# Optimization experiments

Measured on AMD Instinct MI355X. Metric: run time of the kernel, lower is better.

## Reference

```python
import jax, jax.numpy as jnp
import numpy as np
import math

D_MODEL = 1024
N_HEADS = 16
HEAD_DIM = D_MODEL // N_HEADS  # 64
R = HEAD_DIM // 2              # 32
ROPE_BASE = 10000.0
B, T = 4, 2048


def setup_inputs() -> dict:
    key = jax.random.key(0)
    k1, k2, k3, k4, k5 = jax.random.split(key, 5)
    x = jax.random.normal(k1, (B, T, D_MODEL), dtype=jnp.float32)
    Wqkv = jax.random.normal(k2, (3 * D_MODEL, D_MODEL), dtype=jnp.float32) * (1.0 / math.sqrt(D_MODEL))
    Wout = jax.random.normal(k3, (D_MODEL, D_MODEL), dtype=jnp.float32) * (1.0 / math.sqrt(D_MODEL))
    alpha = jax.random.normal(k4, (N_HEADS, R), dtype=jnp.float32) * 0.01
    beta = jax.random.normal(k5, (N_HEADS, R), dtype=jnp.float32) * 0.01
    return {"x": x, "Wqkv": Wqkv, "Wout": Wout, "alpha": alpha, "beta": beta}


def _fourier_bias(alpha, beta, t):
    # omega[r] = base^{-2r/head_dim}, same geometric spacing as RoPE
    omega = ROPE_BASE ** (-2.0 * jnp.arange(R, dtype=jnp.float32) / HEAD_DIM)
    # bias depends only on displacement i-j in [-(t-1), t-1]: compute once per
    # displacement, then gather into the (t, t) matrix (same math as full T x T).
    disp = jnp.arange(-(t - 1), t, dtype=jnp.float32)            # (2t-1,)
    angles = omega[:, None] * disp[None, :]                       # (R, 2t-1)
    vec = jnp.einsum('hr,rk->hk', alpha, jnp.cos(angles)) \
        + jnp.einsum('hr,rk->hk', beta, jnp.sin(angles))          # (H, 2t-1)
    i = jnp.arange(t)
    idx = i[:, None] - i[None, :] + (t - 1)                       # (t, t), delta[i,j]=i-j
    return vec[:, idx]                                            # (H, t, t)


def reference(x, Wqkv, Wout, alpha, beta):
    b, t, d = x.shape
    qkv = x @ Wqkv.T                                              # (B, T, 3D)
    q, k, v = jnp.split(qkv, 3, axis=-1)
    def heads(a):
        return a.reshape(b, t, N_HEADS, HEAD_DIM).transpose(0, 2, 1, 3)  # (B,H,T,dh)
    q, k, v = heads(q), heads(k), heads(v)
    scale = 1.0 / math.sqrt(HEAD_DIM)
    logits = jnp.einsum('bhqd,bhkd->bhqk', q, k) * scale          # (B,H,T,T)
    logits = logits + _fourier_bias(alpha, beta, t)[None]
    causal = jnp.tril(jnp.ones((t, t), dtype=bool))
    logits = jnp.where(causal[None, None], logits, -jnp.inf)
    attn = jax.nn.softmax(logits, axis=-1)
    out = jnp.einsum('bhqk,bhkd->bhqd', attn, v)                  # (B,H,T,dh)
    out = out.transpose(0, 2, 1, 3).reshape(b, t, d)
    return out @ Wout.T
```

## Files before the change

kernel.cpp:

```cpp
#include <hip/hip_runtime.h>
#include <cstdint>
#include <cstddef>

typedef _Float16 f16;
typedef f16 f16x8 __attribute__((ext_vector_type(8)));
typedef __fp16 fp16x2 __attribute__((ext_vector_type(2)));
typedef float f32x4 __attribute__((ext_vector_type(4)));
typedef float f32x16 __attribute__((ext_vector_type(16)));
typedef uint32_t u32;


__device__ __forceinline__ void gload16(const void* g, void* l) {
  __builtin_amdgcn_global_load_lds((const __attribute__((address_space(1))) void*)g,
                                   (__attribute__((address_space(3))) void*)l,
                                   16u, 0, 0u);
}

__device__ __forceinline__ u32 pkrtz(float a, float b) {
  union { fp16x2 v; u32 u; } t;
  t.v = __builtin_amdgcn_cvt_pkrtz(a, b);
  return t.u;
}

__device__ __forceinline__ u32 packh2(float a, float b) { return pkrtz(a, b); }

__device__ __forceinline__ float max3f(float a, float b, float c) {
  return fmaxf(fmaxf(a, b), c);
}

__device__ __forceinline__ void pl32swap(u32& a, u32& b) {
  asm volatile("v_permlane32_swap_b32 %0, %1" : "+v"(a), "+v"(b));
}


__global__ __launch_bounds__(256) void cvt_f32_f16(const float* __restrict__ in,
                                                   f16* __restrict__ out, int n) {
  int i = (blockIdx.x * 256 + threadIdx.x) * 8;
  if (i >= n) return;
  float4 a = *(const float4*)(in + i);
  float4 b = *(const float4*)(in + i + 4);
  f16x8 o;
  o[0] = (f16)a.x; o[1] = (f16)a.y; o[2] = (f16)a.z; o[3] = (f16)a.w;
  o[4] = (f16)b.x; o[5] = (f16)b.y; o[6] = (f16)b.z; o[7] = (f16)b.w;
  *(f16x8*)(out + i) = o;
}


__global__ __launch_bounds__(256) void build_tables(const float* __restrict__ alpha,
                                                    const float* __restrict__ beta,
                                                    f16* __restrict__ U,
                                                    f16* __restrict__ Wt) {
  int idx = blockIdx.x * 256 + threadIdx.x;
  int t = idx >> 5, r = idx & 31;
  float w = powf(10000.0f, -(float)r / 32.0f);
  float ang = w * (float)t;
  float c = cosf(ang), s = sinf(ang);
  const float L2E = 1.44269504089f;
  U[t * 64 + 2 * r]     = (f16)(c * L2E);
  U[t * 64 + 2 * r + 1] = (f16)(s * L2E);
  #pragma unroll
  for (int h = 0; h < 16; ++h) {
    float al = alpha[h * 32 + r], be = beta[h * 32 + r];
    Wt[(size_t)(h * 2048 + t) * 64 + 2 * r]     = (f16)(al * c - be * s);
    Wt[(size_t)(h * 2048 + t) * 64 + 2 * r + 1] = (f16)(al * s + be * c);
  }
}


__global__ __launch_bounds__(256) void gemm_qkv(const f16* __restrict__ A,
                                                const f16* __restrict__ B,
                                                f16* __restrict__ Q,
                                                f16* __restrict__ Kh,
                                                f16* __restrict__ Vt) {
  __shared__ __align__(16) char sm[65536];
  const int K = 1024;
  int tid = threadIdx.x;
  int lane = tid & 63, wid = tid >> 6;
  int bid = blockIdx.x;
  int xcd = bid & 7;
  int id = bid >> 3;
  int nl = id / 64;
  int m0 = (id & 63) * 128;
  int n0 = (xcd * 3 + nl) * 128;
  int wm = wid >> 1, wn = wid & 1;
  int c = lane & 15, g = lane >> 4, l7 = lane & 7;

  int srow[4], sce[4], sdst[4];
  #pragma unroll
  for (int i = 0; i < 4; ++i) {
    int p = i * 4096 + tid * 16;
    int q = p ^ (((p >> 7) & 7) << 4);
    srow[i] = q >> 7; sce[i] = (q & 127) >> 1;
    sdst[i] = i * 4096 + wid * 1024;
  }

  f32x4 acc[4][4] = {};

  #pragma unroll
  for (int i = 0; i < 4; ++i) {
    gload16(A + (size_t)(m0 + srow[i]) * K + sce[i], sm + sdst[i]);
    gload16(B + (size_t)(n0 + srow[i]) * K + sce[i], sm + 32768 + sdst[i]);
  }
  __syncthreads();

  for (int kt = 0; kt < 16; ++kt) {
    int cur = kt & 1;
    char* As = sm + cur * 16384;
    char* Bs = sm + 32768 + cur * 16384;

    if (kt < 15) {
      char* Ad = sm + (cur ^ 1) * 16384;
      char* Bd = sm + 32768 + (cur ^ 1) * 16384;
      #pragma unroll
      for (int i = 0; i < 4; ++i) {
        gload16(A + (size_t)(m0 + srow[i]) * K + (kt + 1) * 64 + sce[i], Ad + sdst[i]);
        gload16(B + (size_t)(n0 + srow[i]) * K + (kt + 1) * 64 + sce[i], Bd + sdst[i]);
      }
    }

    __builtin_amdgcn_s_setprio(1);
    #pragma unroll
    for (int kk = 0; kk < 2; ++kk) {
      int co = (kk * 64 + g * 16) ^ (l7 << 4);
      f16x8 af[4], bf[4];
      #pragma unroll
      for (int fr = 0; fr < 4; ++fr)
        af[fr] = *(const f16x8*)(As + (wm * 64 + fr * 16 + c) * 128 + co);
      #pragma unroll
      for (int fn = 0; fn < 4; ++fn)
        bf[fn] = *(const f16x8*)(Bs + (wn * 64 + fn * 16 + c) * 128 + co);
      #pragma unroll
      for (int fr = 0; fr < 4; ++fr)
        #pragma unroll
        for (int fn = 0; fn < 4; ++fn)
          acc[fr][fn] = __builtin_amdgcn_mfma_f32_16x16x32_f16(af[fr], bf[fn], acc[fr][fn], 0, 0, 0);
    }
    __builtin_amdgcn_s_setprio(0);
    __syncthreads();
  }

  int which = n0 >> 10;
  #pragma unroll
  for (int fr = 0; fr < 4; ++fr) {
    int m = m0 + wm * 64 + fr * 16 + g * 4;
    int b = m >> 11, t = m & 2047;
    #pragma unroll
    for (int fn = 0; fn < 4; ++fn) {
      int n = n0 + wn * 64 + fn * 16 + c;
      int nf = n & 1023, hh = nf >> 6, d = nf & 63;
      if (which == 0) {
        #pragma unroll
        for (int r = 0; r < 4; ++r)
          Q[(size_t)((b * 16 + hh) * 2048 + (t + r)) * 64 + d] = (f16)(acc[fr][fn][r] * 0.180336880111f);
      } else if (which == 1) {
        #pragma unroll
        for (int r = 0; r < 4; ++r)
          Kh[(size_t)((b * 16 + hh) * 2048 + (t + r)) * 64 + d] = (f16)acc[fr][fn][r];
      } else {
        uint2 pk;
        pk.x = packh2(acc[fr][fn][0], acc[fr][fn][1]);
        pk.y = packh2(acc[fr][fn][2], acc[fr][fn][3]);
        *(uint2*)(Vt + (size_t)((b * 16 + hh) * 64 + d) * 2048 + t) = pk;
      }
    }
  }
}


__global__ __launch_bounds__(256) void gemm_out(const f16* __restrict__ A,
                                                const f16* __restrict__ B,
                                                float* __restrict__ Cout) {
  __shared__ __align__(16) char sm[65536];
  const int K = 1024;
  int tid = threadIdx.x;
  int lane = tid & 63, wid = tid >> 6;
  int bid = blockIdx.x;
  int xcd = bid & 7;
  int id = bid >> 3;
  int m0 = id * 128;
  int n0 = xcd * 128;
  int wm = wid >> 1, wn = wid & 1;
  int c = lane & 15, g = lane >> 4, l7 = lane & 7;

  int srow[4], sce[4], sdst[4];
  #pragma unroll
  for (int i = 0; i < 4; ++i) {
    int p = i * 4096 + tid * 16;
    int q = p ^ (((p >> 7) & 7) << 4);
    srow[i] = q >> 7; sce[i] = (q & 127) >> 1;
    sdst[i] = i * 4096 + wid * 1024;
  }

  f32x4 acc[4][4] = {};

  #pragma unroll
  for (int i = 0; i < 4; ++i) {
    gload16(A + (size_t)(m0 + srow[i]) * K + sce[i], sm + sdst[i]);
    gload16(B + (size_t)(n0 + srow[i]) * K + sce[i], sm + 32768 + sdst[i]);
  }
  __syncthreads();

  for (int kt = 0; kt < 16; ++kt) {
    int cur = kt & 1;
    char* As = sm + cur * 16384;
    char* Bs = sm + 32768 + cur * 16384;

    if (kt < 15) {
      char* Ad = sm + (cur ^ 1) * 16384;
      char* Bd = sm + 32768 + (cur ^ 1) * 16384;
      #pragma unroll
      for (int i = 0; i < 4; ++i) {
        gload16(A + (size_t)(m0 + srow[i]) * K + (kt + 1) * 64 + sce[i], Ad + sdst[i]);
        gload16(B + (size_t)(n0 + srow[i]) * K + (kt + 1) * 64 + sce[i], Bd + sdst[i]);
      }
    }

    __builtin_amdgcn_s_setprio(1);
    #pragma unroll
    for (int kk = 0; kk < 2; ++kk) {
      int co = (kk * 64 + g * 16) ^ (l7 << 4);
      f16x8 af[4], bf[4];
      #pragma unroll
      for (int fr = 0; fr < 4; ++fr)
        af[fr] = *(const f16x8*)(As + (wm * 64 + fr * 16 + c) * 128 + co);
      #pragma unroll
      for (int fn = 0; fn < 4; ++fn)
        bf[fn] = *(const f16x8*)(Bs + (wn * 64 + fn * 16 + c) * 128 + co);
      #pragma unroll
      for (int fr = 0; fr < 4; ++fr)
        #pragma unroll
        for (int fn = 0; fn < 4; ++fn)
          acc[fr][fn] = __builtin_amdgcn_mfma_f32_16x16x32_f16(af[fr], bf[fn], acc[fr][fn], 0, 0, 0);
    }
    __builtin_amdgcn_s_setprio(0);
    __syncthreads();
  }

  #pragma unroll
  for (int fr = 0; fr < 4; ++fr) {
    int m = m0 + wm * 64 + fr * 16 + g * 4;
    #pragma unroll
    for (int fn = 0; fn < 4; ++fn) {
      int n = n0 + wn * 64 + fn * 16 + c;
      #pragma unroll
      for (int r = 0; r < 4; ++r)
        Cout[(size_t)(m + r) * 1024 + n] = acc[fr][fn][r];
    }
  }
}


__global__ __launch_bounds__(512, 2) void attn(const f16* __restrict__ Q,
                                               const f16* __restrict__ Kh,
                                               const f16* __restrict__ Vt,
                                               const f16* __restrict__ U,
                                               const f16* __restrict__ Wt,
                                               f16* __restrict__ AO) {
  __shared__ __align__(16) char sm[98304];
  int tid = threadIdx.x, lane = tid & 63, wid = tid >> 6;
  int l31 = lane & 31, hi = lane >> 5;
  int o = blockIdx.x;
  int pr = o >> 6;
  int bh = o & 63;
  int h = bh & 15, b = bh >> 4;
  int swz = (lane & 15) << 4;

  const f16* ksrc[4]; int kdst[4];
  #pragma unroll
  for (int i = 0; i < 4; ++i) {
    int p = i * 8192 + tid * 16;
    int row = p >> 8;
    int col = (p & 255) ^ ((row & 15) << 4);
    int ce = col >> 1;
    ksrc[i] = (ce < 64) ? (Kh + (size_t)(bh * 2048 + row) * 64 + ce)
                        : (Wt + (size_t)(h * 2048 + row) * 64 + (ce - 64));
    kdst[i] = i * 8192 + wid * 1024;
  }
  const f16* vsrc[2]; int vdst[2];
  #pragma unroll
  for (int i = 0; i < 2; ++i) {
    int p = i * 8192 + tid * 16;
    int row = p >> 8;
    int col = (p & 255) ^ ((row & 15) << 4);
    int ce = col >> 1;
    vsrc[i] = Vt + (size_t)(bh * 64 + row) * 2048 + ce;
    vdst[i] = i * 8192 + wid * 1024;
  }

  #pragma unroll 1
  for (int pass = 0; pass < 2; ++pass) {
    int qt = pass ? pr : 7 - pr;
    int qrow = qt * 256 + wid * 32 + l31;
    int ktmax = 2 * qt + 1;

    f16x8 qf[8];
    {
      const f16* qp = Q + (size_t)(bh * 2048 + qrow) * 64 + hi * 8;
      const f16* up = U + (size_t)qrow * 64 + hi * 8;
      #pragma unroll
      for (int ks = 0; ks < 4; ++ks) {
        qf[ks]     = *(const f16x8*)(qp + ks * 16);
        qf[4 + ks] = *(const f16x8*)(up + ks * 16);
      }
    }

    float m_i = -1e30f, l_i = 0.0f;
    f32x16 accA = {}, accB = {};

    #pragma unroll
    for (int i = 0; i < 4; ++i) gload16(ksrc[i], sm + kdst[i]);
    #pragma unroll
    for (int i = 0; i < 2; ++i) gload16(vsrc[i], sm + 65536 + vdst[i]);
    __syncthreads();

    for (int kt = 0; kt <= ktmax; ++kt) {
      int cur = kt & 1;
      char* Ks = sm + cur * 32768;
      char* Vs = sm + 65536 + cur * 16384;

      if (kt < ktmax) {
        char* kb = sm + (cur ^ 1) * 32768;
        char* vb = sm + 65536 + (cur ^ 1) * 16384;
        #pragma unroll
        for (int i = 0; i < 4; ++i) gload16(ksrc[i] + (size_t)(kt + 1) * 8192, kb + kdst[i]);
        #pragma unroll
        for (int i = 0; i < 2; ++i) gload16(vsrc[i] + (size_t)(kt + 1) * 128, vb + vdst[i]);
      }

      f32x16 st0 = {}, st1 = {}, st2 = {}, st3 = {};
      __builtin_amdgcn_s_setprio(1);
      #pragma unroll
      for (int ks = 0; ks < 8; ++ks) {
        int co = (ks * 32 + hi * 16) ^ swz;
        f16x8 k0 = *(const f16x8*)(Ks + l31 * 256 + co);
        f16x8 k1 = *(const f16x8*)(Ks + (32 + l31) * 256 + co);
        f16x8 k2 = *(const f16x8*)(Ks + (64 + l31) * 256 + co);
        f16x8 k3 = *(const f16x8*)(Ks + (96 + l31) * 256 + co);
        st0 = __builtin_amdgcn_mfma_f32_32x32x16_f16(k0, qf[ks], st0, 0, 0, 0);
        st1 = __builtin_amdgcn_mfma_f32_32x32x16_f16(k1, qf[ks], st1, 0, 0, 0);
        st2 = __builtin_amdgcn_mfma_f32_32x32x16_f16(k2, qf[ks], st2, 0, 0, 0);
        st3 = __builtin_amdgcn_mfma_f32_32x32x16_f16(k3, qf[ks], st3, 0, 0, 0);
      }
      __builtin_amdgcn_s_setprio(0);

      int kv0 = kt * 128;
      if (kv0 + 127 > qt * 256 + wid * 32) {
        #pragma unroll
        for (int r = 0; r < 16; ++r) {
          int kvl = kv0 + (r & 3) + 8 * (r >> 2) + 4 * hi;
          if (kvl > qrow) st0[r] = -1e30f;
          if (kvl + 32 > qrow) st1[r] = -1e30f;
          if (kvl + 64 > qrow) st2[r] = -1e30f;
          if (kvl + 96 > qrow) st3[r] = -1e30f;
        }
      }

      float pm = fmaxf(fmaxf(st0[0], st1[0]), fmaxf(st2[0], st3[0]));
      #pragma unroll
      for (int r = 1; r < 16; ++r) {
        pm = max3f(pm, st0[r], st1[r]);
        pm = max3f(pm, st2[r], st3[r]);
      }
      pm = fmaxf(pm, __shfl_xor(pm, 32, 64));
      if (!__all(pm <= m_i + 8.0f)) {
        float mnew = fmaxf(m_i, pm);
        float sc = __builtin_amdgcn_exp2f(m_i - mnew);
        l_i *= sc;
        accA *= sc;
        accB *= sc;
        m_i = mnew;
      }

      float ps = 0.0f;
      u32 pk0[8], pk1[8], pk2[8], pk3[8];
      #pragma unroll
      for (int j = 0; j < 8; ++j) {
        float a0 = __builtin_amdgcn_exp2f(st0[2 * j] - m_i);
        float a1 = __builtin_amdgcn_exp2f(st0[2 * j + 1] - m_i);
        float b0 = __builtin_amdgcn_exp2f(st1[2 * j] - m_i);
        float b1 = __builtin_amdgcn_exp2f(st1[2 * j + 1] - m_i);
        float c0 = __builtin_amdgcn_exp2f(st2[2 * j] - m_i);
        float c1 = __builtin_amdgcn_exp2f(st2[2 * j + 1] - m_i);
        float d0 = __builtin_amdgcn_exp2f(st3[2 * j] - m_i);
        float d1 = __builtin_amdgcn_exp2f(st3[2 * j + 1] - m_i);
        ps += (a0 + a1) + (b0 + b1) + (c0 + c1) + (d0 + d1);
        pk0[j] = pkrtz(a0, a1);
        pk1[j] = pkrtz(b0, b1);
        pk2[j] = pkrtz(c0, c1);
        pk3[j] = pkrtz(d0, d1);
      }
      ps += __shfl_xor(ps, 32, 64);
      l_i += ps;

      pl32swap(pk0[0], pk0[2]); pl32swap(pk0[1], pk0[3]);
      pl32swap(pk0[4], pk0[6]); pl32swap(pk0[5], pk0[7]);
      pl32swap(pk1[0], pk1[2]); pl32swap(pk1[1], pk1[3]);
      pl32swap(pk1[4], pk1[6]); pl32swap(pk1[5], pk1[7]);
      pl32swap(pk2[0], pk2[2]); pl32swap(pk2[1], pk2[3]);
      pl32swap(pk2[4], pk2[6]); pl32swap(pk2[5], pk2[7]);
      pl32swap(pk3[0], pk3[2]); pl32swap(pk3[1], pk3[3]);
      pl32swap(pk3[4], pk3[6]); pl32swap(pk3[5], pk3[7]);

      __builtin_amdgcn_s_setprio(1);
      #pragma unroll
      for (int kb = 0; kb < 8; ++kb) {
        union { u32 w[4]; f16x8 v; } bf;
        const u32* pk = (kb < 2) ? pk0 : (kb < 4) ? pk1 : (kb < 6) ? pk2 : pk3;
        int base = (kb & 1) * 4;
        bf.w[0] = pk[base + 0]; bf.w[1] = pk[base + 1];
        bf.w[2] = pk[base + 2]; bf.w[3] = pk[base + 3];
        int co = (kb * 32 + hi * 16) ^ swz;
        f16x8 v0 = *(const f16x8*)(Vs + l31 * 256 + co);
        f16x8 v1 = *(const f16x8*)(Vs + (32 + l31) * 256 + co);
        accA = __builtin_amdgcn_mfma_f32_32x32x16_f16(v0, bf.v, accA, 0, 0, 0);
        accB = __builtin_amdgcn_mfma_f32_32x32x16_f16(v1, bf.v, accB, 0, 0, 0);
      }
      __builtin_amdgcn_s_setprio(0);
      __syncthreads();
    }

    float inv = __builtin_amdgcn_rcpf(l_i);
    f16* aop = AO + (size_t)(b * 2048 + qrow) * 1024 + h * 64;
    #pragma unroll
    for (int u = 0; u < 4; ++u) {
      uint2 ov;
      ov.x = pkrtz(accA[4 * u] * inv, accA[4 * u + 1] * inv);
      ov.y = pkrtz(accA[4 * u + 2] * inv, accA[4 * u + 3] * inv);
      *(uint2*)(aop + 8 * u + 4 * hi) = ov;
      ov.x = pkrtz(accB[4 * u] * inv, accB[4 * u + 1] * inv);
      ov.y = pkrtz(accB[4 * u + 2] * inv, accB[4 * u + 3] * inv);
      *(uint2*)(aop + 32 + 8 * u + 4 * hi) = ov;
    }
  }
}


extern "C" void kernel_launch(void* const* d_in, const int* in_sizes, int n_in,
                              void* d_out, int out_size, void* d_ws, size_t ws_size,
                              hipStream_t stream) {
  const float* x     = (const float*)d_in[0];
  const float* Wqkv  = (const float*)d_in[1];
  const float* Wout  = (const float*)d_in[2];
  const float* alpha = (const float*)d_in[3];
  const float* beta  = (const float*)d_in[4];

  char* ws = (char*)d_ws;
  f16* Xh    = (f16*)(ws);
  f16* Wqkvh = (f16*)(ws + 16777216);
  f16* Wouth = (f16*)(ws + 23068672);
  f16* Qh    = (f16*)(ws + 25165824);
  f16* Kh    = (f16*)(ws + 41943040);
  f16* Vt    = (f16*)(ws + 58720256);
  f16* U     = (f16*)(ws + 75497472);
  f16* Wt    = (f16*)(ws + 75759616);
  f16* AO    = Xh;

  cvt_f32_f16<<<4096, 256, 0, stream>>>(x, Xh, 8388608);
  cvt_f32_f16<<<1536, 256, 0, stream>>>(Wqkv, Wqkvh, 3145728);
  cvt_f32_f16<<<512, 256, 0, stream>>>(Wout, Wouth, 1048576);
  build_tables<<<256, 256, 0, stream>>>(alpha, beta, U, Wt);
  gemm_qkv<<<1536, 256, 0, stream>>>(Xh, Wqkvh, Qh, Kh, Vt);
  attn<<<256, 512, 0, stream>>>(Qh, Kh, Vt, U, Wt, AO);
  gemm_out<<<512, 256, 0, stream>>>(AO, Wouth, (float*)d_out);
}
```

Measured before the change: 185.1 us.

## Use 256x128 tiles with triple-buffered LDS pipeline in both projection GEMMs

Both projection GEMMs now run 512-thread blocks that each compute a 256x128 output tile, which halves the grid sizes. The LDS staging changes from a double buffer with a full barrier every k-step to a three-stage ring. Prefetches run two k-tiles ahead, and an explicit vmcnt wait plus a single barrier replaces __syncthreads. Global-to-LDS loads are split into two groups interleaved with the two MFMA half-steps, to hide memory latency and cut barrier stalls. The 144KB of LDS per block limits each CU to one block, despite the launch-bounds hint of two, so latency hiding relies on the deeper pipeline.

```diff
diff --git a/kernel.cpp b/kernel.cpp
--- a/kernel.cpp
+++ b/kernel.cpp
@@ -67,61 +67,76 @@
 }
 
 
-__global__ __launch_bounds__(256) void gemm_qkv(const f16* __restrict__ A,
-                                                const f16* __restrict__ B,
-                                                f16* __restrict__ Q,
-                                                f16* __restrict__ Kh,
-                                                f16* __restrict__ Vt) {
-  __shared__ __align__(16) char sm[65536];
+
+__global__ __launch_bounds__(512, 2) void gemm_qkv(const f16* __restrict__ A,
+                                                   const f16* __restrict__ B,
+                                                   f16* __restrict__ Q,
+                                                   f16* __restrict__ Kh,
+                                                   f16* __restrict__ Vt) {
+  __shared__ __align__(16) char sm[147456];
   const int K = 1024;
   int tid = threadIdx.x;
   int lane = tid & 63, wid = tid >> 6;
   int bid = blockIdx.x;
   int xcd = bid & 7;
-  int id = bid >> 3;
-  int nl = id / 64;
-  int m0 = (id & 63) * 128;
+  int loc = bid >> 3;
+  int nl = loc >> 5;
+  int m0 = (loc & 31) * 256;
   int n0 = (xcd * 3 + nl) * 128;
   int wm = wid >> 1, wn = wid & 1;
-  int c = lane & 15, g = lane >> 4, l7 = lane & 7;
-
-  int srow[4], sce[4], sdst[4];
+  int c = lane & 15, g = lane >> 4;
+  int swz = (c & 7) << 4;
+
+  const f16* asrc[4]; int adst[4];
   #pragma unroll
   for (int i = 0; i < 4; ++i) {
-    int p = i * 4096 + tid * 16;
-    int q = p ^ (((p >> 7) & 7) << 4);
-    srow[i] = q >> 7; sce[i] = (q & 127) >> 1;
-    sdst[i] = i * 4096 + wid * 1024;
+    int p = i * 8192 + tid * 16;
+    int row = p >> 7;
+    int col = (p & 127) ^ ((row & 7) << 4);
+    asrc[i] = A + (size_t)(m0 + row) * K + (col >> 1);
+    adst[i] = i * 8192 + wid * 1024;
+  }
+  const f16* bsrc[2]; int bdst[2];
+  #pragma unroll
+  for (int i = 0; i < 2; ++i) {
+    int p = i * 8192 + tid * 16;
+    int row = p >> 7;
+    int col = (p & 127) ^ ((row & 7) << 4);
+    bsrc[i] = B + (size_t)(n0 + row) * K + (col >> 1);
+    bdst[i] = i * 8192 + wid * 1024;
   }
 
   f32x4 acc[4][4] = {};
 
   #pragma unroll
-  for (int i = 0; i < 4; ++i) {
-    gload16(A + (size_t)(m0 + srow[i]) * K + sce[i], sm + sdst[i]);
-    gload16(B + (size_t)(n0 + srow[i]) * K + sce[i], sm + 32768 + sdst[i]);
-  }
-  __syncthreads();
+  for (int i = 0; i < 4; ++i) gload16(asrc[i], sm + adst[i]);
+  #pragma unroll
+  for (int i = 0; i < 2; ++i) gload16(bsrc[i], sm + 98304 + bdst[i]);
+  #pragma unroll
+  for (int i = 0; i < 4; ++i) gload16(asrc[i] + 64, sm + 32768 + adst[i]);
+  #pragma unroll
+  for (int i = 0; i < 2; ++i) gload16(bsrc[i] + 64, sm + 98304 + 16384 + bdst[i]);
 
   for (int kt = 0; kt < 16; ++kt) {
-    int cur = kt & 1;
-    char* As = sm + cur * 16384;
-    char* Bs = sm + 32768 + cur * 16384;
-
-    if (kt < 15) {
-      char* Ad = sm + (cur ^ 1) * 16384;
-      char* Bd = sm + 32768 + (cur ^ 1) * 16384;
-      #pragma unroll
-      for (int i = 0; i < 4; ++i) {
-        gload16(A + (size_t)(m0 + srow[i]) * K + (kt + 1) * 64 + sce[i], Ad + sdst[i]);
-        gload16(B + (size_t)(n0 + srow[i]) * K + (kt + 1) * 64 + sce[i], Bd + sdst[i]);
-      }
-    }
-
-    __builtin_amdgcn_s_setprio(1);
-    #pragma unroll
-    for (int kk = 0; kk < 2; ++kk) {
-      int co = (kk * 64 + g * 16) ^ (l7 << 4);
+    if (kt < 15) asm volatile("s_waitcnt vmcnt(6)" ::: "memory");
+    else         asm volatile("s_waitcnt vmcnt(0)" ::: "memory");
+    __builtin_amdgcn_s_barrier();
+
+    int j = kt % 3;
+    char* As = sm + j * 32768;
+    char* Bs = sm + 98304 + j * 16384;
+    int jn = (kt + 2) % 3;
+    char* Ad = sm + jn * 32768;
+    char* Bd = sm + 98304 + jn * 16384;
+    bool stg = (kt <= 13);
+
+    if (stg) {
+      gload16(asrc[0] + (kt + 2) * 64, Ad + adst[0]);
+      gload16(asrc[1] + (kt + 2) * 64, Ad + adst[1]);
+      gload16(asrc[2] + (kt + 2) * 64, Ad + adst[2]);
+    }
+    {
+      int co = (g * 16) ^ swz;
       f16x8 af[4], bf[4];
       #pragma unroll
       for (int fr = 0; fr < 4; ++fr)
@@ -129,14 +144,36 @@
       #pragma unroll
       for (int fn = 0; fn < 4; ++fn)
         bf[fn] = *(const f16x8*)(Bs + (wn * 64 + fn * 16 + c) * 128 + co);
+      __builtin_amdgcn_s_setprio(1);
       #pragma unroll
       for (int fr = 0; fr < 4; ++fr)
         #pragma unroll
         for (int fn = 0; fn < 4; ++fn)
           acc[fr][fn] = __builtin_amdgcn_mfma_f32_16x16x32_f16(af[fr], bf[fn], acc[fr][fn], 0, 0, 0);
-    }
-    __builtin_amdgcn_s_setprio(0);
-    __syncthreads();
+      __builtin_amdgcn_s_setprio(0);
+    }
+    if (stg) {
+      gload16(asrc[3] + (kt + 2) * 64, Ad + adst[3]);
+      gload16(bsrc[0] + (kt + 2) * 64, Bd + bdst[0]);
+      gload16(bsrc[1] + (kt + 2) * 64, Bd + bdst[1]);
+    }
+    {
+      int co = (64 + g * 16) ^ swz;
+      f16x8 af[4], bf[4];
+      #pragma unroll
+      for (int fr = 0; fr < 4; ++fr)
+        af[fr] = *(const f16x8*)(As + (wm * 64 + fr * 16 + c) * 128 + co);
+      #pragma unroll
+      for (int fn = 0; fn < 4; ++fn)
+        bf[fn] = *(const f16x8*)(Bs + (wn * 64 + fn * 16 + c) * 128 + co);
+      __builtin_amdgcn_s_setprio(1);
+      #pragma unroll
+      for (int fr = 0; fr < 4; ++fr)
+        #pragma unroll
+        for (int fn = 0; fn < 4; ++fn)
+          acc[fr][fn] = __builtin_amdgcn_mfma_f32_16x16x32_f16(af[fr], bf[fn], acc[fr][fn], 0, 0, 0);
+      __builtin_amdgcn_s_setprio(0);
+    }
   }
 
   int which = n0 >> 10;
@@ -167,58 +204,72 @@
 }
 
 
-__global__ __launch_bounds__(256) void gemm_out(const f16* __restrict__ A,
-                                                const f16* __restrict__ B,
-                                                float* __restrict__ Cout) {
-  __shared__ __align__(16) char sm[65536];
+__global__ __launch_bounds__(512, 2) void gemm_out(const f16* __restrict__ A,
+                                                   const f16* __restrict__ B,
+                                                   float* __restrict__ Cout) {
+  __shared__ __align__(16) char sm[147456];
   const int K = 1024;
   int tid = threadIdx.x;
   int lane = tid & 63, wid = tid >> 6;
   int bid = blockIdx.x;
   int xcd = bid & 7;
-  int id = bid >> 3;
-  int m0 = id * 128;
+  int loc = bid >> 3;
+  int m0 = loc * 256;
   int n0 = xcd * 128;
   int wm = wid >> 1, wn = wid & 1;
-  int c = lane & 15, g = lane >> 4, l7 = lane & 7;
-
-  int srow[4], sce[4], sdst[4];
+  int c = lane & 15, g = lane >> 4;
+  int swz = (c & 7) << 4;
+
+  const f16* asrc[4]; int adst[4];
   #pragma unroll
   for (int i = 0; i < 4; ++i) {
-    int p = i * 4096 + tid * 16;
-    int q = p ^ (((p >> 7) & 7) << 4);
-    srow[i] = q >> 7; sce[i] = (q & 127) >> 1;
-    sdst[i] = i * 4096 + wid * 1024;
+    int p = i * 8192 + tid * 16;
+    int row = p >> 7;
+    int col = (p & 127) ^ ((row & 7) << 4);
+    asrc[i] = A + (size_t)(m0 + row) * K + (col >> 1);
+    adst[i] = i * 8192 + wid * 1024;
+  }
+  const f16* bsrc[2]; int bdst[2];
+  #pragma unroll
+  for (int i = 0; i < 2; ++i) {
+    int p = i * 8192 + tid * 16;
+    int row = p >> 7;
+    int col = (p & 127) ^ ((row & 7) << 4);
+    bsrc[i] = B + (size_t)(n0 + row) * K + (col >> 1);
+    bdst[i] = i * 8192 + wid * 1024;
   }
 
   f32x4 acc[4][4] = {};
 
   #pragma unroll
-  for (int i = 0; i < 4; ++i) {
-    gload16(A + (size_t)(m0 + srow[i]) * K + sce[i], sm + sdst[i]);
-    gload16(B + (size_t)(n0 + srow[i]) * K + sce[i], sm + 32768 + sdst[i]);
-  }
-  __syncthreads();
+  for (int i = 0; i < 4; ++i) gload16(asrc[i], sm + adst[i]);
+  #pragma unroll
+  for (int i = 0; i < 2; ++i) gload16(bsrc[i], sm + 98304 + bdst[i]);
+  #pragma unroll
+  for (int i = 0; i < 4; ++i) gload16(asrc[i] + 64, sm + 32768 + adst[i]);
+  #pragma unroll
+  for (int i = 0; i < 2; ++i) gload16(bsrc[i] + 64, sm + 98304 + 16384 + bdst[i]);
 
   for (int kt = 0; kt < 16; ++kt) {
-    int cur = kt & 1;
-    char* As = sm + cur * 16384;
-    char* Bs = sm + 32768 + cur * 16384;
-
-    if (kt < 15) {
-      char* Ad = sm + (cur ^ 1) * 16384;
-      char* Bd = sm + 32768 + (cur ^ 1) * 16384;
-      #pragma unroll
-      for (int i = 0; i < 4; ++i) {
-        gload16(A + (size_t)(m0 + srow[i]) * K + (kt + 1) * 64 + sce[i], Ad + sdst[i]);
-        gload16(B + (size_t)(n0 + srow[i]) * K + (kt + 1) * 64 + sce[i], Bd + sdst[i]);
-      }
-    }
-
-    __builtin_amdgcn_s_setprio(1);
-    #pragma unroll
-    for (int kk = 0; kk < 2; ++kk) {
-      int co = (kk * 64 + g * 16) ^ (l7 << 4);
+    if (kt < 15) asm volatile("s_waitcnt vmcnt(6)" ::: "memory");
+    else         asm volatile("s_waitcnt vmcnt(0)" ::: "memory");
+    __builtin_amdgcn_s_barrier();
+
+    int j = kt % 3;
+    char* As = sm + j * 32768;
+    char* Bs = sm + 98304 + j * 16384;
+    int jn = (kt + 2) % 3;
+    char* Ad = sm + jn * 32768;
+    char* Bd = sm + 98304 + jn * 16384;
+    bool stg = (kt <= 13);
+
+    if (stg) {
+      gload16(asrc[0] + (kt + 2) * 64, Ad + adst[0]);
+      gload16(asrc[1] + (kt + 2) * 64, Ad + adst[1]);
+      gload16(asrc[2] + (kt + 2) * 64, Ad + adst[2]);
+    }
+    {
+      int co = (g * 16) ^ swz;
       f16x8 af[4], bf[4];
       #pragma unroll
       for (int fr = 0; fr < 4; ++fr)
@@ -226,14 +277,36 @@
       #pragma unroll
       for (int fn = 0; fn < 4; ++fn)
         bf[fn] = *(const f16x8*)(Bs + (wn * 64 + fn * 16 + c) * 128 + co);
+      __builtin_amdgcn_s_setprio(1);
       #pragma unroll
       for (int fr = 0; fr < 4; ++fr)
         #pragma unroll
         for (int fn = 0; fn < 4; ++fn)
           acc[fr][fn] = __builtin_amdgcn_mfma_f32_16x16x32_f16(af[fr], bf[fn], acc[fr][fn], 0, 0, 0);
-    }
-    __builtin_amdgcn_s_setprio(0);
-    __syncthreads();
+      __builtin_amdgcn_s_setprio(0);
+    }
+    if (stg) {
+      gload16(asrc[3] + (kt + 2) * 64, Ad + adst[3]);
+      gload16(bsrc[0] + (kt + 2) * 64, Bd + bdst[0]);
+      gload16(bsrc[1] + (kt + 2) * 64, Bd + bdst[1]);
+    }
+    {
+      int co = (64 + g * 16) ^ swz;
+      f16x8 af[4], bf[4];
+      #pragma unroll
+      for (int fr = 0; fr < 4; ++fr)
+        af[fr] = *(const f16x8*)(As + (wm * 64 + fr * 16 + c) * 128 + co);
+      #pragma unroll
+      for (int fn = 0; fn < 4; ++fn)
+        bf[fn] = *(const f16x8*)(Bs + (wn * 64 + fn * 16 + c) * 128 + co);
+      __builtin_amdgcn_s_setprio(1);
+      #pragma unroll
+      for (int fr = 0; fr < 4; ++fr)
+        #pragma unroll
+        for (int fn = 0; fn < 4; ++fn)
+          acc[fr][fn] = __builtin_amdgcn_mfma_f32_16x16x32_f16(af[fr], bf[fn], acc[fr][fn], 0, 0, 0);
+      __builtin_amdgcn_s_setprio(0);
+    }
   }
 
   #pragma unroll
@@ -459,7 +532,7 @@
   cvt_f32_f16<<<1536, 256, 0, stream>>>(Wqkv, Wqkvh, 3145728);
   cvt_f32_f16<<<512, 256, 0, stream>>>(Wout, Wouth, 1048576);
   build_tables<<<256, 256, 0, stream>>>(alpha, beta, U, Wt);
-  gemm_qkv<<<1536, 256, 0, stream>>>(Xh, Wqkvh, Qh, Kh, Vt);
+  gemm_qkv<<<768, 512, 0, stream>>>(Xh, Wqkvh, Qh, Kh, Vt);
   attn<<<256, 512, 0, stream>>>(Qh, Kh, Vt, U, Wt, AO);
-  gemm_out<<<512, 256, 0, stream>>>(AO, Wouth, (float*)d_out);
-}
+  gemm_out<<<256, 512, 0, stream>>>(AO, Wouth, (float*)d_out);
+}
```

New measurement: 192.2 us. 3.8% more time.
